# Optimization experiments

Measured on AMD Instinct MI355X. Metric: run time of the kernel, lower is better.

## Reference

```python
import jax, jax.numpy as jnp
import numpy as np

RADIUS = 4
NUM_LEVELS = 4
STRIDES = (1, 1, 1, 1)


def _level_corr(f1, f2, coords, r, stride):
    """Windowed bilinear correlation at one pyramid level.
    f1: [B,C,H,W] (full-res features), f2: [B,C,H2,W2] (level features),
    coords: [B,2,H,W] (x,y) already scaled to f2's resolution.
    Returns [B,(2r+1)^2,H,W].
    """
    B, C, H, W = f1.shape
    H2, W2 = f2.shape[2], f2.shape[3]
    f1t = jnp.transpose(f1, (0, 2, 3, 1))                     # [B,H,W,C]
    f2f = jnp.transpose(f2, (0, 2, 3, 1)).reshape(B, H2 * W2, C)
    d = jnp.arange(-r, r + 1, dtype=f1.dtype) * stride
    dy, dx = jnp.meshgrid(d, d, indexing='ij')
    deltas = jnp.stack([dx.ravel(), dy.ravel()], axis=-1)      # [(2r+1)^2, 2]

    def one_offset(delta):
        x = coords[:, 0] + delta[0]                            # [B,H,W]
        y = coords[:, 1] + delta[1]
        x0 = jnp.floor(x)
        y0 = jnp.floor(y)
        acc = jnp.zeros((B, H, W), f1.dtype)
        # 4 bilinear corners, zero padding outside the feature map
        for cx in (0.0, 1.0):
            for cy in (0.0, 1.0):
                xc = x0 + cx
                yc = y0 + cy
                w = (1.0 - jnp.abs(x - xc)) * (1.0 - jnp.abs(y - yc))
                valid = (xc >= 0) & (xc <= W2 - 1) & (yc >= 0) & (yc <= H2 - 1)
                idx = (jnp.clip(yc, 0, H2 - 1) * W2 + jnp.clip(xc, 0, W2 - 1)).astype(jnp.int32)
                g = jax.vmap(lambda t, i: t[i])(f2f, idx.reshape(B, -1)).reshape(B, H, W, C)
                acc = acc + jnp.where(valid, w, 0.0) * jnp.einsum('bhwc,bhwc->bhw', f1t, g)
        return acc                                             # [B,H,W]

    corr = jax.lax.map(one_offset, deltas)                     # [K,B,H,W]
    return jnp.transpose(corr, (1, 0, 2, 3))                   # [B,K,H,W]


def _corr_block(fmap1, fmap2s, coords):
    C = fmap1.shape[1]
    outs = []
    for i, f2 in enumerate(fmap2s):
        outs.append(_level_corr(fmap1, f2, coords / (2.0 ** i), RADIUS, STRIDES[i]))
    corr = jnp.concatenate(outs, axis=1)                       # [B, L*(2r+1)^2, H, W]
    return corr / jnp.sqrt(jnp.asarray(C, fmap1.dtype))


def setup_inputs() -> dict:
    key = jax.random.key(0)
    ks = jax.random.split(key, 6)
    B, C, H, W = 2, 256, 64, 64
    inp = {'fmap1': jax.random.normal(ks[0], (B, C, H, W), jnp.float32)}
    for i in range(NUM_LEVELS):
        h, w = H >> i, W >> i
        inp['fmap2_%d' % i] = jax.random.normal(ks[1 + i], (B, C, h, w), jnp.float32)
    gy, gx = jnp.meshgrid(jnp.arange(H, dtype=jnp.float32), jnp.arange(W, dtype=jnp.float32), indexing='ij')
    base = jnp.broadcast_to(jnp.stack([gx, gy], 0)[None], (B, 2, H, W))
    flow = 2.0 * jax.random.normal(jax.random.fold_in(key, 99), (B, 2, H, W), jnp.float32)
    inp['coords'] = base + flow
    return inp


def reference(fmap1, fmap2_0, fmap2_1, fmap2_2, fmap2_3, coords):
    return _corr_block(fmap1, [fmap2_0, fmap2_1, fmap2_2, fmap2_3], coords)
```

## Files before the change

kernel.cpp:

```cpp
#include <hip/hip_runtime.h>

#define RADIUS 4
#define KK 81
#define HWP 4096

typedef _Float16 f16x8 __attribute__((ext_vector_type(8)));
typedef float    f32x4 __attribute__((ext_vector_type(4)));

#define OFF_F1T  0u
#define OFF_L0   4194304u
#define OFF_L1   8388608u
#define OFF_L2   9437184u
#define OFF_L3   9699328u
#define OFF_ZPAD 9764864u
#define OFF_END  9765376u

__global__ __launch_bounds__(256) void stage_kernel(
    const float* __restrict__ f1, const float* __restrict__ l0,
    const float* __restrict__ l1, const float* __restrict__ l2,
    const float* __restrict__ l3, char* __restrict__ wsB)
{
    __shared__ float tile[32][33];
    const int bx = blockIdx.x;
    const int b  = blockIdx.z;
    const int r0 = blockIdx.y * 32;
    const int tx = threadIdx.x, ty = threadIdx.y;
    if (bx == 0 && blockIdx.y == 0 && b == 0) {
        const int tt = ty * 32 + tx;
        if (tt < 128) ((float*)(wsB + OFF_ZPAD))[tt] = 0.0f;
    }
    const float* src; _Float16* dst; int S, s0i;
    if (bx < 128)      { src = f1; dst = (_Float16*)(wsB + OFF_F1T); S = 4096; s0i = bx; }
    else if (bx < 256) { src = l0; dst = (_Float16*)(wsB + OFF_L0);  S = 4096; s0i = bx - 128; }
    else if (bx < 288) { src = l1; dst = (_Float16*)(wsB + OFF_L1);  S = 1024; s0i = bx - 256; }
    else if (bx < 296) { src = l2; dst = (_Float16*)(wsB + OFF_L2);  S = 256;  s0i = bx - 288; }
    else               { src = l3; dst = (_Float16*)(wsB + OFF_L3);  S = 64;   s0i = bx - 296; }
    const int s0 = s0i * 32;
    src += (size_t)b * 256 * S;
    dst += (size_t)b * S * 256;
    #pragma unroll
    for (int i = 0; i < 32; i += 8)
        tile[ty + i][tx] = src[(size_t)(r0 + ty + i) * S + s0 + tx];
    __syncthreads();
    #pragma unroll
    for (int i = 0; i < 32; i += 8)
        dst[(size_t)(s0 + ty + i) * 256 + r0 + tx] = (_Float16)tile[tx][ty + i];
}

__global__ __launch_bounds__(256, 3) void corr_mfma_kernel(
    const char* __restrict__ wsB,
    const float* __restrict__ coords,
    float* __restrict__ out)
{
    __shared__ f32x4 sB[2][1024];
    __shared__ float sD[32][106];
    __shared__ int   sIx[32], sIy[32];
    __shared__ float sW[32][4];
    __shared__ int   sBox[5];

    char* sBb = (char*)sB;

    const int bx   = blockIdx.x;
    const int lvl  = blockIdx.y;
    const int tile = ((bx & 7) << 5) | (bx >> 3);
    const int b    = tile >> 7;
    const int t7   = tile & 127;
    const int tr4  = (t7 >> 3) << 2;
    const int tc8  = (t7 & 7) << 3;
    const int t    = threadIdx.x;
    const int l    = t & 63;
    const int wid  = t >> 6;
    const int aset = wid & 1;
    const int half = wid >> 1;

    const int sh = 6 - lvl;
    const int W2 = 1 << sh;

    for (int i = t; i < 32 * 106; i += 256)
        ((float*)sD)[i] = 0.0f;

    if (t < 32) {
        const int hwc = ((tr4 + (t >> 3)) << 6) + tc8 + (t & 7);
        const float sc = 1.0f / (float)(1 << lvl);
        const float xs = coords[((size_t)b * 2 + 0) * HWP + hwc] * sc;
        const float ys = coords[((size_t)b * 2 + 1) * HWP + hwc] * sc;
        const float x0f = floorf(xs), y0f = floorf(ys);
        sIx[t] = (int)x0f; sIy[t] = (int)y0f;
        const float fx = xs - x0f, fy = ys - y0f;
        sW[t][0] = (1.f - fx) * (1.f - fy);
        sW[t][1] = fx * (1.f - fy);
        sW[t][2] = (1.f - fx) * fy;
        sW[t][3] = fx * fy;
    }
    __syncthreads();
    if (t == 0) {
        int rlo = 1 << 20, rhi = -(1 << 20), clo = 1 << 20, chi = -(1 << 20);
        for (int px = 0; px < 32; ++px) {
            rlo = min(rlo, sIy[px]); rhi = max(rhi, sIy[px]);
            clo = min(clo, sIx[px]); chi = max(chi, sIx[px]);
        }
        const int rl = max(rlo - RADIUS, 0);
        const int rh = min(rhi + RADIUS + 1, W2 - 1);
        const int cf = max(clo - RADIUS, 0);
        const int ce = min(chi + RADIUS + 1, W2 - 1);
        const int nr = rh - rl + 1;
        const int nt = (ce >= cf) ? ((ce - cf + 16) >> 4) : 0;
        sBox[0] = rl;
        sBox[1] = cf;
        sBox[2] = nt;
        sBox[3] = (nr > 0) ? nr * nt : 0;
        sBox[4] = 65535 / max(nt, 1) + 1;
    }

    const int pxl = (aset << 4) + (l & 15);
    const int hwA = ((tr4 + (pxl >> 3)) << 6) + tc8 + (pxl & 7);
    const char* ap = wsB + OFF_F1T + ((size_t)(b * HWP + hwA)) * 512 + ((l >> 4) << 4);
    const f16x8 a0 = __builtin_bit_cast(f16x8, *(const f32x4*)(ap));
    const f16x8 a1 = __builtin_bit_cast(f16x8, *(const f32x4*)(ap + 64));
    const f16x8 a2 = __builtin_bit_cast(f16x8, *(const f32x4*)(ap + 128));
    const f16x8 a3 = __builtin_bit_cast(f16x8, *(const f32x4*)(ap + 192));
    const f16x8 a4 = __builtin_bit_cast(f16x8, *(const f32x4*)(ap + 256));
    const f16x8 a5 = __builtin_bit_cast(f16x8, *(const f32x4*)(ap + 320));
    const f16x8 a6 = __builtin_bit_cast(f16x8, *(const f32x4*)(ap + 384));
    const f16x8 a7 = __builtin_bit_cast(f16x8, *(const f32x4*)(ap + 448));
    __syncthreads();

    const int rlo = sBox[0], cfi = sBox[1], ntw = sBox[2];
    const int ntot = sBox[3], inv = sBox[4];
    const int NP = (ntot + 1) >> 1;
    const unsigned lvbase = ((lvl == 0) ? OFF_L0 : (lvl == 1) ? OFF_L1
                           : (lvl == 2) ? OFF_L2 : OFF_L3)
                          + (((unsigned)b << (2 * sh)) << 9);
    const int coff = l & 15;

    const int pxg  = (aset << 4) + ((l >> 4) << 2);
    const int iy0r = sIy[pxg + 0], ix0r = sIx[pxg + 0];
    const int iy1r = sIy[pxg + 1], ix1r = sIx[pxg + 1];
    const int iy2r = sIy[pxg + 2], ix2r = sIx[pxg + 2];
    const int iy3r = sIy[pxg + 3], ix3r = sIx[pxg + 3];

#define LOADP(P_, R0_, R1_, R2_, R3_) { \
        const int u_ = ((P_) << 1) + (t >> 7); \
        const unsigned q_ = ((unsigned)(u_ * inv)) >> 16; \
        const int j_ = u_ - (int)q_ * ntw; \
        const int col_ = cfi + (j_ << 4) + (t & 15); \
        const bool ok_ = (u_ < ntot) && ((unsigned)col_ < (unsigned)W2); \
        const int row_ = rlo + (int)q_; \
        const char* gp_ = wsB + (ok_ ? (lvbase + ((unsigned)((row_ << sh) + col_) << 9)) \
                                     : OFF_ZPAD) + ((unsigned)((t >> 4) & 7) << 6); \
        R0_ = *(const f32x4*)(gp_); \
        R1_ = *(const f32x4*)(gp_ + 16); \
        R2_ = *(const f32x4*)(gp_ + 32); \
        R3_ = *(const f32x4*)(gp_ + 48); \
        __builtin_amdgcn_sched_barrier(0); }

#define WRITEP(BUF_, R0_, R1_, R2_, R3_) { \
        char* wp_ = sBb + ((BUF_) << 14) + ((t >> 7) << 13) + (((t >> 4) & 7) << 10) \
                  + ((t & 15) << 4); \
        *(f32x4*)(wp_)       = R0_; \
        *(f32x4*)(wp_ + 256) = R1_; \
        *(f32x4*)(wp_ + 512) = R2_; \
        *(f32x4*)(wp_ + 768) = R3_; }

#define CONSUMEP(BUF_, P_) { \
        const int u_ = ((P_) << 1) + half; \
        if (u_ < ntot) { \
            const unsigned q_ = ((unsigned)(u_ * inv)) >> 16; \
            const int j_ = u_ - (int)q_ * ntw; \
            const int row_ = rlo + (int)q_; \
            const char* lb_ = sBb + ((BUF_) << 14) + (half << 13) + ((l >> 4) << 8) \
                            + ((l & 15) << 4); \
            const f16x8 b0_ = __builtin_bit_cast(f16x8, *(const f32x4*)(lb_)); \
            const f16x8 b1_ = __builtin_bit_cast(f16x8, *(const f32x4*)(lb_ + 1024)); \
            const f16x8 b2_ = __builtin_bit_cast(f16x8, *(const f32x4*)(lb_ + 2048)); \
            const f16x8 b3_ = __builtin_bit_cast(f16x8, *(const f32x4*)(lb_ + 3072)); \
            const f16x8 b4_ = __builtin_bit_cast(f16x8, *(const f32x4*)(lb_ + 4096)); \
            const f16x8 b5_ = __builtin_bit_cast(f16x8, *(const f32x4*)(lb_ + 5120)); \
            const f16x8 b6_ = __builtin_bit_cast(f16x8, *(const f32x4*)(lb_ + 6144)); \
            const f16x8 b7_ = __builtin_bit_cast(f16x8, *(const f32x4*)(lb_ + 7168)); \
            f32x4 ac0 = {0.f, 0.f, 0.f, 0.f}; \
            f32x4 ac1 = {0.f, 0.f, 0.f, 0.f}; \
            __builtin_amdgcn_s_setprio(1); \
            ac0 = __builtin_amdgcn_mfma_f32_16x16x32_f16(a0, b0_, ac0, 0, 0, 0); \
            ac1 = __builtin_amdgcn_mfma_f32_16x16x32_f16(a1, b1_, ac1, 0, 0, 0); \
            ac0 = __builtin_amdgcn_mfma_f32_16x16x32_f16(a2, b2_, ac0, 0, 0, 0); \
            ac1 = __builtin_amdgcn_mfma_f32_16x16x32_f16(a3, b3_, ac1, 0, 0, 0); \
            ac0 = __builtin_amdgcn_mfma_f32_16x16x32_f16(a4, b4_, ac0, 0, 0, 0); \
            ac1 = __builtin_amdgcn_mfma_f32_16x16x32_f16(a5, b5_, ac1, 0, 0, 0); \
            ac0 = __builtin_amdgcn_mfma_f32_16x16x32_f16(a6, b6_, ac0, 0, 0, 0); \
            ac1 = __builtin_amdgcn_mfma_f32_16x16x32_f16(a7, b7_, ac1, 0, 0, 0); \
            __builtin_amdgcn_s_setprio(0); \
            const f32x4 accs = ac0 + ac1; \
            const int col_ = cfi + (j_ << 4) + coff; \
            const int p0 = row_ - iy0r + RADIUS, q0 = col_ - ix0r + RADIUS; \
            if ((unsigned)p0 < 10u && (unsigned)q0 < 10u) sD[pxg + 0][p0 * 10 + q0] = accs[0]; \
            const int p1 = row_ - iy1r + RADIUS, q1 = col_ - ix1r + RADIUS; \
            if ((unsigned)p1 < 10u && (unsigned)q1 < 10u) sD[pxg + 1][p1 * 10 + q1] = accs[1]; \
            const int p2 = row_ - iy2r + RADIUS, q2 = col_ - ix2r + RADIUS; \
            if ((unsigned)p2 < 10u && (unsigned)q2 < 10u) sD[pxg + 2][p2 * 10 + q2] = accs[2]; \
            const int p3 = row_ - iy3r + RADIUS, q3 = col_ - ix3r + RADIUS; \
            if ((unsigned)p3 < 10u && (unsigned)q3 < 10u) sD[pxg + 3][p3 * 10 + q3] = accs[3]; \
        } }

    {
        f32x4 XA, XB, XC, XD, YA, YB, YC, YD;
        if (ntot > 0) {
            LOADP(0, XA, XB, XC, XD);
            if (NP > 1) LOADP(1, YA, YB, YC, YD);
            WRITEP(0, XA, XB, XC, XD);
        }
        __syncthreads();
        if (ntot > 0) {
            int p = 0;
            for (;;) {
                if (p + 2 < NP) LOADP(p + 2, XA, XB, XC, XD);
                CONSUMEP(p & 1, p);
                if (p + 1 < NP) WRITEP((p + 1) & 1, YA, YB, YC, YD);
                __syncthreads();
                if (++p >= NP) break;
                if (p + 2 < NP) LOADP(p + 2, YA, YB, YC, YD);
                CONSUMEP(p & 1, p);
                if (p + 1 < NP) WRITEP((p + 1) & 1, XA, XB, XC, XD);
                __syncthreads();
                if (++p >= NP) break;
            }
        }
    }
#undef LOADP
#undef WRITEP
#undef CONSUMEP
    __syncthreads();

    for (int j = t; j < 32 * KK; j += 256) {
        const int px = j & 31;
        const int k  = j >> 5;
        const int p  = (k * 57) >> 9;
        const int q  = k - p * 9;
        const int bi = p * 10 + q;
        const float* dd = sD[px];
        const float v = (sW[px][0] * dd[bi]      + sW[px][1] * dd[bi + 1] +
                         sW[px][2] * dd[bi + 10] + sW[px][3] * dd[bi + 11]) * 0.0625f;
        const int hwp = ((tr4 + (px >> 3)) << 6) + tc8 + (px & 7);
        out[((size_t)b * 324 + lvl * KK + k) * HWP + hwp] = v;
    }
}

__global__ __launch_bounds__(128) void corr_level_kernel(
    const float* __restrict__ f1, const float* __restrict__ f2,
    const float* __restrict__ coords, float* __restrict__ out,
    int H2, int W2, float scale, int lvl)
{
    __shared__ float sf1[256];
    __shared__ float sDl[100];
    const int pix = blockIdx.x;
    const int b   = pix >> 12;
    const int hw  = pix & 4095;
    const int t   = threadIdx.x;
    for (int c = t; c < 256; c += 128)
        sf1[c] = f1[((size_t)b * 256 + c) * 4096 + hw];
    __syncthreads();
    const float xs = coords[((size_t)b * 2 + 0) * 4096 + hw] * scale;
    const float ys = coords[((size_t)b * 2 + 1) * 4096 + hw] * scale;
    const float x0f = floorf(xs), y0f = floorf(ys);
    const float fx = xs - x0f, fy = ys - y0f;
    const int ix0 = (int)x0f, iy0 = (int)y0f;
    if (t < 100) {
        const int p = t / 10, q = t - p * 10;
        const int row = iy0 - 4 + p, col = ix0 - 4 + q;
        float acc = 0.0f;
        if (row >= 0 && row < H2 && col >= 0 && col < W2) {
            const size_t step = (size_t)H2 * W2;
            const size_t base = (size_t)b * 256 * step + (size_t)row * W2 + col;
            #pragma unroll 4
            for (int c = 0; c < 256; ++c)
                acc += f2[base + (size_t)c * step] * sf1[c];
        }
        sDl[t] = acc;
    }
    __syncthreads();
    if (t < 81) {
        const int p = t / 9, q = t - p * 9;
        const float d00 = sDl[p * 10 + q];
        const float d01 = sDl[p * 10 + q + 1];
        const float d10 = sDl[p * 10 + q + 10];
        const float d11 = sDl[p * 10 + q + 11];
        const float v = (1.0f - fy) * ((1.0f - fx) * d00 + fx * d01)
                      + fy * ((1.0f - fx) * d10 + fx * d11);
        out[((size_t)b * 324 + (size_t)lvl * 81 + t) * 4096 + hw] = v * 0.0625f;
    }
}

extern "C" void kernel_launch(void* const* d_in, const int* in_sizes, int n_in,
                              void* d_out, int out_size, void* d_ws, size_t ws_size,
                              hipStream_t stream) {
    (void)out_size;
    const float* f1     = (const float*)d_in[0];
    const float* f2l[4] = {(const float*)d_in[1], (const float*)d_in[2],
                           (const float*)d_in[3], (const float*)d_in[4]};
    const float* coords = (const float*)d_in[5];

    {
        int nbig = 0;
        for (int i = 0; i < n_in; ++i) {
            const int sz = in_sizes[i];
            if (sz == 2097152) {
                if (nbig == 0) f1 = (const float*)d_in[i];
                else           f2l[0] = (const float*)d_in[i];
                ++nbig;
            }
            else if (sz == 524288) f2l[1] = (const float*)d_in[i];
            else if (sz == 131072) f2l[2] = (const float*)d_in[i];
            else if (sz ==  32768) f2l[3] = (const float*)d_in[i];
            else if (sz ==  16384) coords = (const float*)d_in[i];
        }
    }
    float* out = (float*)d_out;
    char*  wsB = (char*)d_ws;

    if (ws_size >= (size_t)OFF_END) {
        stage_kernel<<<dim3(298, 8, 2), dim3(32, 8, 1), 0, stream>>>(
            f1, f2l[0], f2l[1], f2l[2], f2l[3], wsB);
        corr_mfma_kernel<<<dim3(256, 4, 1), 256, 0, stream>>>(wsB, coords, out);
    } else {
        for (int lvl = 0; lvl < 4; ++lvl) {
            const int W2 = 64 >> lvl;
            const float scale = 1.0f / (float)(1 << lvl);
            corr_level_kernel<<<8192, 128, 0, stream>>>(
                f1, f2l[lvl], coords, out, W2, W2, scale, lvl);
        }
    }
}
```

Measured before the change: 43.97 us.

## Enlarge correlation tile to 8x8 pixels with all four waves sharing each B tile

Each block now covers a 64-pixel (8x8) tile instead of 32 pixels. All four waves consume the same staged 16-column B chunk, one per step, instead of two wave pairs splitting chunks. This is meant to reuse each loaded level-feature chunk across more pixels and cut redundant global and LDS traffic, since neighbouring bounding boxes overlap. In exchange the grid halves to 512 blocks, each block may iterate over a larger bounding box one chunk at a time with more barriers, and occupancy and latency hiding may suffer.

```diff
diff --git a/kernel.cpp b/kernel.cpp
--- a/kernel.cpp
+++ b/kernel.cpp
@@ -52,35 +52,33 @@
     const float* __restrict__ coords,
     float* __restrict__ out)
 {
-    __shared__ f32x4 sB[2][1024];
-    __shared__ float sD[32][106];
-    __shared__ int   sIx[32], sIy[32];
-    __shared__ float sW[32][4];
+    __shared__ f32x4 sB[2][512];
+    __shared__ float sD[64][106];
+    __shared__ int   sIx[64], sIy[64];
+    __shared__ float sW[64][4];
     __shared__ int   sBox[5];
 
     char* sBb = (char*)sB;
 
     const int bx   = blockIdx.x;
     const int lvl  = blockIdx.y;
-    const int tile = ((bx & 7) << 5) | (bx >> 3);
-    const int b    = tile >> 7;
-    const int t7   = tile & 127;
-    const int tr4  = (t7 >> 3) << 2;
-    const int tc8  = (t7 & 7) << 3;
+    const int tile = ((bx & 7) << 4) | (bx >> 3);
+    const int b    = tile >> 6;
+    const int t6   = tile & 63;
+    const int tr8  = (t6 >> 3) << 3;
+    const int tc8  = (t6 & 7) << 3;
     const int t    = threadIdx.x;
     const int l    = t & 63;
     const int wid  = t >> 6;
-    const int aset = wid & 1;
-    const int half = wid >> 1;
 
     const int sh = 6 - lvl;
     const int W2 = 1 << sh;
 
-    for (int i = t; i < 32 * 106; i += 256)
+    for (int i = t; i < 64 * 106; i += 256)
         ((float*)sD)[i] = 0.0f;
 
-    if (t < 32) {
-        const int hwc = ((tr4 + (t >> 3)) << 6) + tc8 + (t & 7);
+    if (t < 64) {
+        const int hwc = ((tr8 + (t >> 3)) << 6) + tc8 + (t & 7);
         const float sc = 1.0f / (float)(1 << lvl);
         const float xs = coords[((size_t)b * 2 + 0) * HWP + hwc] * sc;
         const float ys = coords[((size_t)b * 2 + 1) * HWP + hwc] * sc;
@@ -95,7 +93,7 @@
     __syncthreads();
     if (t == 0) {
         int rlo = 1 << 20, rhi = -(1 << 20), clo = 1 << 20, chi = -(1 << 20);
-        for (int px = 0; px < 32; ++px) {
+        for (int px = 0; px < 64; ++px) {
             rlo = min(rlo, sIy[px]); rhi = max(rhi, sIy[px]);
             clo = min(clo, sIx[px]); chi = max(chi, sIx[px]);
         }
@@ -112,8 +110,8 @@
         sBox[4] = 65535 / max(nt, 1) + 1;
     }
 
-    const int pxl = (aset << 4) + (l & 15);
-    const int hwA = ((tr4 + (pxl >> 3)) << 6) + tc8 + (pxl & 7);
+    const int pxl = (wid << 4) + (l & 15);
+    const int hwA = ((tr8 + (pxl >> 3)) << 6) + tc8 + (pxl & 7);
     const char* ap = wsB + OFF_F1T + ((size_t)(b * HWP + hwA)) * 512 + ((l >> 4) << 4);
     const f16x8 a0 = __builtin_bit_cast(f16x8, *(const f32x4*)(ap));
     const f16x8 a1 = __builtin_bit_cast(f16x8, *(const f32x4*)(ap + 64));
@@ -127,49 +125,42 @@
 
     const int rlo = sBox[0], cfi = sBox[1], ntw = sBox[2];
     const int ntot = sBox[3], inv = sBox[4];
-    const int NP = (ntot + 1) >> 1;
     const unsigned lvbase = ((lvl == 0) ? OFF_L0 : (lvl == 1) ? OFF_L1
                            : (lvl == 2) ? OFF_L2 : OFF_L3)
                           + (((unsigned)b << (2 * sh)) << 9);
     const int coff = l & 15;
 
-    const int pxg  = (aset << 4) + ((l >> 4) << 2);
+    const int pxg  = (wid << 4) + ((l >> 4) << 2);
     const int iy0r = sIy[pxg + 0], ix0r = sIx[pxg + 0];
     const int iy1r = sIy[pxg + 1], ix1r = sIx[pxg + 1];
     const int iy2r = sIy[pxg + 2], ix2r = sIx[pxg + 2];
     const int iy3r = sIy[pxg + 3], ix3r = sIx[pxg + 3];
 
-#define LOADP(P_, R0_, R1_, R2_, R3_) { \
-        const int u_ = ((P_) << 1) + (t >> 7); \
+#define LOADP(P_, R0_, R1_) { \
+        const int u_ = (P_); \
         const unsigned q_ = ((unsigned)(u_ * inv)) >> 16; \
         const int j_ = u_ - (int)q_ * ntw; \
         const int col_ = cfi + (j_ << 4) + (t & 15); \
         const bool ok_ = (u_ < ntot) && ((unsigned)col_ < (unsigned)W2); \
         const int row_ = rlo + (int)q_; \
         const char* gp_ = wsB + (ok_ ? (lvbase + ((unsigned)((row_ << sh) + col_) << 9)) \
-                                     : OFF_ZPAD) + ((unsigned)((t >> 4) & 7) << 6); \
+                                     : OFF_ZPAD) + ((unsigned)(t >> 4) << 5); \
         R0_ = *(const f32x4*)(gp_); \
         R1_ = *(const f32x4*)(gp_ + 16); \
-        R2_ = *(const f32x4*)(gp_ + 32); \
-        R3_ = *(const f32x4*)(gp_ + 48); \
         __builtin_amdgcn_sched_barrier(0); }
 
-#define WRITEP(BUF_, R0_, R1_, R2_, R3_) { \
-        char* wp_ = sBb + ((BUF_) << 14) + ((t >> 7) << 13) + (((t >> 4) & 7) << 10) \
-                  + ((t & 15) << 4); \
+#define WRITEP(BUF_, R0_, R1_) { \
+        char* wp_ = sBb + ((BUF_) << 13) + ((t >> 4) << 9) + ((t & 15) << 4); \
         *(f32x4*)(wp_)       = R0_; \
-        *(f32x4*)(wp_ + 256) = R1_; \
-        *(f32x4*)(wp_ + 512) = R2_; \
-        *(f32x4*)(wp_ + 768) = R3_; }
+        *(f32x4*)(wp_ + 256) = R1_; }
 
 #define CONSUMEP(BUF_, P_) { \
-        const int u_ = ((P_) << 1) + half; \
+        const int u_ = (P_); \
         if (u_ < ntot) { \
             const unsigned q_ = ((unsigned)(u_ * inv)) >> 16; \
             const int j_ = u_ - (int)q_ * ntw; \
             const int row_ = rlo + (int)q_; \
-            const char* lb_ = sBb + ((BUF_) << 14) + (half << 13) + ((l >> 4) << 8) \
-                            + ((l & 15) << 4); \
+            const char* lb_ = sBb + ((BUF_) << 13) + ((l >> 4) << 8) + ((l & 15) << 4); \
             const f16x8 b0_ = __builtin_bit_cast(f16x8, *(const f32x4*)(lb_)); \
             const f16x8 b1_ = __builtin_bit_cast(f16x8, *(const f32x4*)(lb_ + 1024)); \
             const f16x8 b2_ = __builtin_bit_cast(f16x8, *(const f32x4*)(lb_ + 2048)); \
@@ -203,24 +194,25 @@
         } }
 
     {
-        f32x4 XA, XB, XC, XD, YA, YB, YC, YD;
-        if (ntot > 0) {
-            LOADP(0, XA, XB, XC, XD);
-            if (NP > 1) LOADP(1, YA, YB, YC, YD);
-            WRITEP(0, XA, XB, XC, XD);
+        f32x4 XA, XB, YA, YB;
+        const int NP = ntot;
+        if (NP > 0) {
+            LOADP(0, XA, XB);
+            if (NP > 1) LOADP(1, YA, YB);
+            WRITEP(0, XA, XB);
         }
         __syncthreads();
-        if (ntot > 0) {
+        if (NP > 0) {
             int p = 0;
             for (;;) {
-                if (p + 2 < NP) LOADP(p + 2, XA, XB, XC, XD);
+                if (p + 2 < NP) LOADP(p + 2, XA, XB);
                 CONSUMEP(p & 1, p);
-                if (p + 1 < NP) WRITEP((p + 1) & 1, YA, YB, YC, YD);
+                if (p + 1 < NP) WRITEP((p + 1) & 1, YA, YB);
                 __syncthreads();
                 if (++p >= NP) break;
-                if (p + 2 < NP) LOADP(p + 2, YA, YB, YC, YD);
+                if (p + 2 < NP) LOADP(p + 2, YA, YB);
                 CONSUMEP(p & 1, p);
-                if (p + 1 < NP) WRITEP((p + 1) & 1, XA, XB, XC, XD);
+                if (p + 1 < NP) WRITEP((p + 1) & 1, XA, XB);
                 __syncthreads();
                 if (++p >= NP) break;
             }
@@ -231,16 +223,16 @@
 #undef CONSUMEP
     __syncthreads();
 
-    for (int j = t; j < 32 * KK; j += 256) {
-        const int px = j & 31;
-        const int k  = j >> 5;
+    for (int j = t; j < 64 * KK; j += 256) {
+        const int px = j & 63;
+        const int k  = j >> 6;
         const int p  = (k * 57) >> 9;
         const int q  = k - p * 9;
         const int bi = p * 10 + q;
         const float* dd = sD[px];
         const float v = (sW[px][0] * dd[bi]      + sW[px][1] * dd[bi + 1] +
                          sW[px][2] * dd[bi + 10] + sW[px][3] * dd[bi + 11]) * 0.0625f;
-        const int hwp = ((tr4 + (px >> 3)) << 6) + tc8 + (px & 7);
+        const int hwp = ((tr8 + (px >> 3)) << 6) + tc8 + (px & 7);
         out[((size_t)b * 324 + lvl * KK + k) * HWP + hwp] = v;
     }
 }
@@ -320,7 +312,7 @@
     if (ws_size >= (size_t)OFF_END) {
         stage_kernel<<<dim3(298, 8, 2), dim3(32, 8, 1), 0, stream>>>(
             f1, f2l[0], f2l[1], f2l[2], f2l[3], wsB);
-        corr_mfma_kernel<<<dim3(256, 4, 1), 256, 0, stream>>>(wsB, coords, out);
+        corr_mfma_kernel<<<dim3(128, 4, 1), 256, 0, stream>>>(wsB, coords, out);
     } else {
         for (int lvl = 0; lvl < 4; ++lvl) {
             const int W2 = 64 >> lvl;
```

Measured after the change: 46.99 us. 1.07x slower.
